# Kernel tuning notes

Measured on AMD Instinct MI355X. Metric: run time of the kernel, lower is better.

Reference implementation:

```python
import jax, jax.numpy as jnp
import numpy as np

MIN_NEAR = 0.05
DENSITY_SCALE = 1.0
BOUND = 1.0  # spherical scene bounds radius
GEO = 15


def _density_mlp(x, dW1, db1, dW2, db2, dW3, db3):
    h = jax.nn.relu(x @ dW1 + db1)
    h = jax.nn.relu(h @ dW2 + db2)
    h = h @ dW3 + db3  # [M, 1+GEO]
    sigma = jnp.exp(jnp.clip(h[..., 0], -15.0, 15.0))  # trunc_exp
    return sigma, h[..., 1:]


def _color_mlp(d, geo, cW1, cb1, cW2, cb2, cW3, cb3):
    h = jnp.concatenate([d, geo], axis=-1)
    h = jax.nn.relu(h @ cW1 + cb1)
    h = jax.nn.relu(h @ cW2 + cb2)
    return jax.nn.sigmoid(h @ cW3 + cb3)


def _comp_weights(deltas, sigmas):
    # alpha compositing: w_i = alpha_i * prod_{j<i}(1 - alpha_j)
    alphas = 1.0 - jnp.exp(-deltas * sigmas)
    trans = jnp.cumprod(
        jnp.concatenate([jnp.ones_like(alphas[:, :1]), 1.0 - alphas + 1e-15], axis=-1),
        axis=-1)[:, :-1]
    return alphas * trans


def _sample_pdf(bins, weights, n_samples):
    # deterministic importance resampling (eval mode); bins [N,T-1], weights [N,T-2]
    weights = weights + 1e-5
    pdf = weights / jnp.sum(weights, axis=-1, keepdims=True)
    cdf = jnp.cumsum(pdf, axis=-1)
    cdf = jnp.concatenate([jnp.zeros_like(cdf[:, :1]), cdf], axis=-1)  # [N, T-1]
    u = jnp.linspace(0.5 / n_samples, 1.0 - 0.5 / n_samples, n_samples)
    u = jnp.broadcast_to(u, (bins.shape[0], n_samples))
    inds = jax.vmap(lambda c, uu: jnp.searchsorted(c, uu, side='right'))(cdf, u)
    below = jnp.clip(inds - 1, 0, cdf.shape[-1] - 1)
    above = jnp.clip(inds, 0, cdf.shape[-1] - 1)
    cdf_g0 = jnp.take_along_axis(cdf, below, axis=-1)
    cdf_g1 = jnp.take_along_axis(cdf, above, axis=-1)
    bmax = bins.shape[-1] - 1
    bins_g0 = jnp.take_along_axis(bins, jnp.clip(below, 0, bmax), axis=-1)
    bins_g1 = jnp.take_along_axis(bins, jnp.clip(above, 0, bmax), axis=-1)
    denom = jnp.where(cdf_g1 - cdf_g0 < 1e-5, 1.0, cdf_g1 - cdf_g0)
    t = (u - cdf_g0) / denom
    return bins_g0 + t * (bins_g1 - bins_g0)


def _run(rays_o, rays_d, dW1, db1, dW2, db2, dW3, db3,
         cW1, cb1, cW2, cb2, cW3, cb3, num_steps, upsample_steps):
    N = rays_o.shape[0]
    # get_z_val_bounds: ray/sphere intersection, sphere radius BOUND at origin
    b = jnp.sum(rays_o * rays_d, axis=-1)
    c = jnp.sum(rays_o * rays_o, axis=-1) - BOUND ** 2
    disc = jnp.maximum(b * b - c, 0.0)
    z_max = jnp.maximum(-b + jnp.sqrt(disc), MIN_NEAR + 1e-3)
    z_min = jnp.full_like(z_max, MIN_NEAR)
    # get_foreground_z_vals: per-ray linspace (perturb=False)
    t = jnp.linspace(0.0, 1.0, num_steps)
    z_vals = z_min[:, None] + (z_max - z_min)[:, None] * t[None, :]
    z_vals = jnp.clip(z_vals, z_min[:, None], z_max[:, None])
    xyzs = rays_o[:, None, :] + rays_d[:, None, :] * z_vals[..., None]
    sigma, geo = _density_mlp(xyzs.reshape(-1, 3), dW1, db1, dW2, db2, dW3, db3)
    sigma = sigma.reshape(N, num_steps)
    geo = geo.reshape(N, num_steps, GEO)

    # upsample_z_values: importance resampling from coarse weights
    deltas = z_vals[:, 1:] - z_vals[:, :-1]
    aug = jnp.concatenate([deltas, deltas[:, -1:]], axis=-1)
    w_coarse = _comp_weights(aug, DENSITY_SCALE * sigma)
    z_mid = 0.5 * (z_vals[:, :-1] + z_vals[:, 1:])
    new_z = jax.lax.stop_gradient(_sample_pdf(z_mid, w_coarse[:, 1:-1], upsample_steps))
    new_xyzs = rays_o[:, None, :] + rays_d[:, None, :] * new_z[..., None]
    new_sigma, new_geo = _density_mlp(new_xyzs.reshape(-1, 3), dW1, db1, dW2, db2, dW3, db3)
    new_sigma = new_sigma.reshape(N, upsample_steps)
    new_geo = new_geo.reshape(N, upsample_steps, GEO)

    # sort/gather merge of coarse + fine samples
    z_all = jnp.concatenate([z_vals, new_z], axis=1)
    order = jnp.argsort(z_all, axis=1)
    z_vals = jnp.take_along_axis(z_all, order, axis=1)  # [N, T]
    xyzs = jnp.take_along_axis(jnp.concatenate([xyzs, new_xyzs], axis=1), order[..., None], axis=1)
    sigma = jnp.take_along_axis(jnp.concatenate([sigma, new_sigma], axis=1), order, axis=1)
    geo = jnp.take_along_axis(jnp.concatenate([geo, new_geo], axis=1), order[..., None], axis=1)

    deltas = z_vals[:, 1:] - z_vals[:, :-1]
    aug = jnp.concatenate([deltas, deltas[:, -1:]], axis=-1)
    weights = _comp_weights(aug, DENSITY_SCALE * sigma)  # [N, T]

    mask = weights > 1e-4
    dirs = jnp.broadcast_to(rays_d[:, None, :], xyzs.shape).reshape(-1, 3)
    rgb = _color_mlp(dirs, geo.reshape(-1, GEO), cW1, cb1, cW2, cb2, cW3, cb3)
    rgbs = jnp.where(mask.reshape(-1, 1), rgb, 0.0).reshape(N, -1, 3)

    weights_sum = jnp.sum(weights, axis=-1)
    depth = jnp.sum(weights * z_vals, axis=-1)
    image = jnp.sum(weights[..., None] * rgbs, axis=-2)
    bg = 206.0 / 255.0
    image = image + (1.0 - weights_sum)[..., None] * bg

    # pairwise distortion loss (the (z_shifted - z_shifted) term in the source is identically zero)
    sample_dist = 1.0 / num_steps
    z_shift = jnp.concatenate([z_vals[:, 1:], jnp.full((N, 1), sample_dist, z_vals.dtype)], axis=-1)
    mid_zs = 0.5 * z_vals + 0.5 * z_shift
    pair = jnp.abs(mid_zs[:, None, :] - mid_zs[:, :, None]) * (weights[:, None, :] * weights[:, :, None])
    loss = jnp.sum(pair, axis=(1, 2)) / (depth + 1e-6)
    loss = jnp.where(loss < 1e-3, 0.0, loss)  # cutoff
    return jnp.concatenate([image, depth[:, None], loss[:, None]], axis=-1)  # [N, 5]


def setup_inputs() -> dict:
    key = jax.random.key(0)
    ks = jax.random.split(key, 16)
    N, H = 2048, 256
    rays_o = 0.1 * jax.random.normal(ks[0], (N, 3), jnp.float32)  # near scene centre
    rd = jax.random.normal(ks[1], (N, 3), jnp.float32)
    rays_d = rd / jnp.linalg.norm(rd, axis=-1, keepdims=True)

    def w(k, shape):
        return jax.random.normal(k, shape, jnp.float32) * (1.0 / np.sqrt(shape[0]))

    return {
        'rays_o': rays_o, 'rays_d': rays_d,
        'dW1': w(ks[2], (3, H)), 'db1': jnp.zeros(H, jnp.float32),
        'dW2': w(ks[3], (H, H)), 'db2': jnp.zeros(H, jnp.float32),
        'dW3': w(ks[4], (H, 1 + GEO)), 'db3': jnp.zeros(1 + GEO, jnp.float32),
        'cW1': w(ks[5], (3 + GEO, H)), 'cb1': jnp.zeros(H, jnp.float32),
        'cW2': w(ks[6], (H, H)), 'cb2': jnp.zeros(H, jnp.float32),
        'cW3': w(ks[7], (H, 3)), 'cb3': jnp.zeros(3, jnp.float32),
        'num_steps': 128, 'upsample_steps': 128,
    }


def reference(rays_o, rays_d, dW1, db1, dW2, db2, dW3, db3,
              cW1, cb1, cW2, cb2, cW3, cb3, num_steps, upsample_steps):
    return _run(rays_o, rays_d, dW1, db1, dW2, db2, dW3, db3,
                cW1, cb1, cW2, cb2, cW3, cb3, num_steps, upsample_steps)
```

## Files before the change

kernel.cpp:

```cpp
#include <hip/hip_runtime.h>


typedef float f32x4 __attribute__((ext_vector_type(4)));
typedef __bf16 bf16x8 __attribute__((ext_vector_type(8)));
typedef __bf16 bf16x4 __attribute__((ext_vector_type(4)));
typedef unsigned short u16x8 __attribute__((ext_vector_type(8)));
typedef unsigned short u16x4 __attribute__((ext_vector_type(4)));

#define NRAYS 2048
#define NSTEP 128
#define TSAMP 256
#define MIN_NEAR 0.05f
#define DTPW 4

#define OFF_D1 0
#define OFF_D2 8192
#define OFF_D3 73728
#define OFF_C1 77824
#define OFF_C2 86016
#define OFF_C3 151552
#define PACK_TOTAL 155648

__device__ __forceinline__ unsigned short f2bf(float f) {
  __bf16 h = (__bf16)f;
  return __builtin_bit_cast(unsigned short, h);
}
__device__ __forceinline__ u16x4 pack4(float a, float b, float c, float d) {
  bf16x4 h;
  h[0] = (__bf16)a; h[1] = (__bf16)b; h[2] = (__bf16)c; h[3] = (__bf16)d;
  return __builtin_bit_cast(u16x4, h);
}

__device__ __forceinline__ float ray_z(const float* __restrict__ ro,
                                       const float* __restrict__ rd, int r, int i) {
  float ox = ro[r * 3], oy = ro[r * 3 + 1], oz = ro[r * 3 + 2];
  float dx = rd[r * 3], dy = rd[r * 3 + 1], dz = rd[r * 3 + 2];
  float b = ox * dx + oy * dy + oz * dz;
  float c = ox * ox + oy * oy + oz * oz - 1.0f;
  float disc = fmaxf(b * b - c, 0.0f);
  float zmax = fmaxf(-b + sqrtf(disc), MIN_NEAR + 1e-3f);
  float zmin = MIN_NEAR;
  float tt = (float)i / 127.0f;
  float zz = zmin + (zmax - zmin) * tt;
  return fminf(fmaxf(zz, zmin), zmax);
}

__device__ __forceinline__ void pack_std(const float* __restrict__ W,
                                         unsigned short* __restrict__ dst,
                                         int idx, int K, int Norig, int NT) {
  int per = NT * 512;
  int kt = idx / per, rm = idx % per;
  int nt = rm >> 9, lane = (rm >> 3) & 63, j = rm & 7;
  int k = kt * 32 + ((lane >> 4) << 3) + j;
  int n = nt * 16 + (lane & 15);
  float v = (k < K && n < Norig) ? W[k * Norig + n] : 0.0f;
  dst[idx] = f2bf(v);
}

__global__ void k_pack_all(const float* __restrict__ dW1, const float* __restrict__ dW2,
                           const float* __restrict__ dW3, const float* __restrict__ cW1,
                           const float* __restrict__ cW2, const float* __restrict__ cW3,
                           unsigned short* __restrict__ Wp) {
  int idx = blockIdx.x * 256 + threadIdx.x;
  if (idx < OFF_D2) {
    pack_std(dW1, Wp + OFF_D1, idx - OFF_D1, 3, 256, 16);
  } else if (idx < OFF_D3) {
    pack_std(dW2, Wp + OFF_D2, idx - OFF_D2, 256, 256, 16);
  } else if (idx < OFF_C1) {
    int j2 = idx - OFF_D3;
    int lane = (j2 >> 3) & 63, jj = j2 & 7, kt = j2 >> 9;
    int k = kt * 32 + ((lane >> 4) << 3) + jj;
    int n = lane & 15;
    Wp[idx] = f2bf(dW3[k * 16 + ((n + 1) & 15)]);
  } else if (idx < OFF_C2) {
    int j2 = idx - OFF_C1;
    int nt = j2 >> 9, lane = (j2 >> 3) & 63, jj = j2 & 7;
    int k = ((lane >> 4) << 3) + jj;
    int n = nt * 16 + (lane & 15);
    float v = 0.0f;
    if (k < 15) v = cW1[(3 + k) * 256 + n];
    else if (k >= 16 && k < 19) v = cW1[(k - 16) * 256 + n];
    Wp[idx] = f2bf(v);
  } else if (idx < OFF_C3) {
    pack_std(cW2, Wp + OFF_C2, idx - OFF_C2, 256, 256, 16);
  } else if (idx < PACK_TOTAL) {
    pack_std(cW3, Wp + OFF_C3, idx - OFF_C3, 256, 3, 1);
  }
}


__device__ __forceinline__ void mlp_l1(const unsigned short* xb, unsigned short* buf,
                                       const bf16x8 (&w1r)[4], const float* sb1,
                                       int wid, int quad, int col) {
#pragma unroll
  for (int h = 0; h < 2; ++h) {
    f32x4 acc[8];
#pragma unroll
    for (int i = 0; i < 8; ++i) acc[i] = (f32x4){0.f, 0.f, 0.f, 0.f};
    int p0 = (h * 2) * 16 + col, p1 = (h * 2 + 1) * 16 + col;
    bf16x8 x0 = *reinterpret_cast<const bf16x8*>(&xb[p0 * 32 + ((quad ^ (p0 & 3)) * 8)]);
    bf16x8 x1 = *reinterpret_cast<const bf16x8*>(&xb[p1 * 32 + ((quad ^ (p1 & 3)) * 8)]);
#pragma unroll
    for (int ntl = 0; ntl < 4; ++ntl) {
      acc[ntl * 2 + 0] = __builtin_amdgcn_mfma_f32_16x16x32_bf16(w1r[ntl], x0, acc[ntl * 2 + 0], 0, 0, 0);
      acc[ntl * 2 + 1] = __builtin_amdgcn_mfma_f32_16x16x32_bf16(w1r[ntl], x1, acc[ntl * 2 + 1], 0, 0, 0);
    }
#pragma unroll
    for (int ntl = 0; ntl < 4; ++ntl) {
      int n = (wid * 4 + ntl) * 16 + quad * 4;
      f32x4 bv = *reinterpret_cast<const f32x4*>(&sb1[n]);
#pragma unroll
      for (int j = 0; j < 2; ++j) {
        int p = (h * 2 + j) * 16 + col;
        *reinterpret_cast<u16x4*>(&buf[p * 256 + (((n >> 3) ^ (p & 31)) * 8) + (n & 7)]) =
            pack4(fmaxf(acc[ntl * 2 + j][0] + bv[0], 0.0f),
                  fmaxf(acc[ntl * 2 + j][1] + bv[1], 0.0f),
                  fmaxf(acc[ntl * 2 + j][2] + bv[2], 0.0f),
                  fmaxf(acc[ntl * 2 + j][3] + bv[3], 0.0f));
      }
    }
  }
}

__device__ __forceinline__ void l2_half_compute(const unsigned short* buf,
                                                const bf16x8 (&w2r)[8][4],
                                                f32x4 (&acc)[8], int h, int quad, int col) {
#pragma unroll
  for (int i = 0; i < 8; ++i) acc[i] = (f32x4){0.f, 0.f, 0.f, 0.f};
#pragma unroll
  for (int kt = 0; kt < 8; ++kt) {
    int p0 = (h * 2) * 16 + col, p1 = (h * 2 + 1) * 16 + col;
    bf16x8 x0 = *reinterpret_cast<const bf16x8*>(&buf[p0 * 256 + (((kt * 4 + quad) ^ (p0 & 31)) * 8)]);
    bf16x8 x1 = *reinterpret_cast<const bf16x8*>(&buf[p1 * 256 + (((kt * 4 + quad) ^ (p1 & 31)) * 8)]);
#pragma unroll
    for (int ntl = 0; ntl < 4; ++ntl) {
      acc[ntl * 2 + 0] = __builtin_amdgcn_mfma_f32_16x16x32_bf16(w2r[kt][ntl], x0, acc[ntl * 2 + 0], 0, 0, 0);
      acc[ntl * 2 + 1] = __builtin_amdgcn_mfma_f32_16x16x32_bf16(w2r[kt][ntl], x1, acc[ntl * 2 + 1], 0, 0, 0);
    }
  }
}

__device__ __forceinline__ void l2_half_write(unsigned short* buf, const f32x4 (&acc)[8],
                                              const float* sb2, int h, int wid, int quad, int col) {
#pragma unroll
  for (int ntl = 0; ntl < 4; ++ntl) {
    int n = (wid * 4 + ntl) * 16 + quad * 4;
    f32x4 bv = *reinterpret_cast<const f32x4*>(&sb2[n]);
#pragma unroll
    for (int j = 0; j < 2; ++j) {
      int p = (h * 2 + j) * 16 + col;
      *reinterpret_cast<u16x4*>(&buf[p * 256 + (((n >> 3) ^ (p & 31)) * 8) + (n & 7)]) =
          pack4(fmaxf(acc[ntl * 2 + j][0] + bv[0], 0.0f),
                fmaxf(acc[ntl * 2 + j][1] + bv[1], 0.0f),
                fmaxf(acc[ntl * 2 + j][2] + bv[2], 0.0f),
                fmaxf(acc[ntl * 2 + j][3] + bv[3], 0.0f));
    }
  }
}

template <bool FIRST>
__global__ __launch_bounds__(256, 2)
void k_density(const float* __restrict__ ro, const float* __restrict__ rd,
               const float* __restrict__ zin,
               const unsigned short* __restrict__ Wp1, const float* __restrict__ b1,
               const unsigned short* __restrict__ Wp2, const float* __restrict__ b2,
               const unsigned short* __restrict__ Wp3, const float* __restrict__ b3,
               unsigned short* __restrict__ gout, float* __restrict__ sig,
               float* __restrict__ z_f) {
  __shared__ __align__(16) unsigned short buf[64 * 256];
  __shared__ unsigned short xb[64 * 32];
  __shared__ unsigned short sW3[4096];
  __shared__ __align__(16) float sb1[256];
  __shared__ __align__(16) float sb2[256];
  __shared__ float sb3[16];
  __shared__ float ssig[256];
  const int t = threadIdx.x;
  const int lane = t & 63, wid = t >> 6, quad = lane >> 4, col = lane & 15;
  const int p_ = t >> 2, g_ = t & 3;

  sb1[t] = b1[t];
  sb2[t] = b2[t];
  if (t < 16) sb3[t] = b3[(t + 1) & 15];
  { const u16x8* s = (const u16x8*)Wp3; u16x8* d = (u16x8*)sW3;
    d[t] = s[t]; d[t + 256] = s[t + 256]; }

  bf16x8 w1r[4], w2r[8][4];
#pragma unroll
  for (int ntl = 0; ntl < 4; ++ntl)
    w1r[ntl] = *reinterpret_cast<const bf16x8*>(Wp1 + ((wid * 4 + ntl) * 64 + lane) * 8);
#pragma unroll
  for (int kt = 0; kt < 8; ++kt)
#pragma unroll
    for (int ntl = 0; ntl < 4; ++ntl)
      w2r[kt][ntl] = *reinterpret_cast<const bf16x8*>(Wp2 + ((kt * 16 + wid * 4 + ntl) * 64 + lane) * 8);

#pragma unroll 1
  for (int tt = 0; tt < DTPW; ++tt) {
    const int P0 = blockIdx.x * 256 + tt * 64;
    {
      u16x8 pk = {0, 0, 0, 0, 0, 0, 0, 0};
      if (g_ == 0) {
        int P = P0 + p_;
        int rr_ = P >> 7, ii = P & 127;
        float zz;
        if constexpr (FIRST) zz = ray_z(ro, rd, rr_, ii);
        else zz = zin[P];
        pk[0] = f2bf(ro[rr_ * 3 + 0] + rd[rr_ * 3 + 0] * zz);
        pk[1] = f2bf(ro[rr_ * 3 + 1] + rd[rr_ * 3 + 1] * zz);
        pk[2] = f2bf(ro[rr_ * 3 + 2] + rd[rr_ * 3 + 2] * zz);
      }
      *reinterpret_cast<u16x8*>(&xb[p_ * 32 + ((g_ ^ (p_ & 3)) * 8)]) = pk;
    }
    __syncthreads();
    mlp_l1(xb, buf, w1r, sb1, wid, quad, col);
    __syncthreads();
    f32x4 acc[8];
    l2_half_compute(buf, w2r, acc, 0, quad, col);
    __syncthreads();
    l2_half_write(buf, acc, sb2, 0, wid, quad, col);
    l2_half_compute(buf, w2r, acc, 1, quad, col);
    __syncthreads();
    l2_half_write(buf, acc, sb2, 1, wid, quad, col);
    __syncthreads();
    {
      const int p = wid * 16 + col;
      f32x4 a3 = {0.f, 0.f, 0.f, 0.f};
#pragma unroll
      for (int kt = 0; kt < 8; ++kt) {
        bf16x8 w = *reinterpret_cast<const bf16x8*>(&sW3[(kt * 64 + lane) * 8]);
        bf16x8 x = *reinterpret_cast<const bf16x8*>(&buf[p * 256 + (((kt * 4 + quad) ^ (p & 31)) * 8)]);
        a3 = __builtin_amdgcn_mfma_f32_16x16x32_bf16(w, x, a3, 0, 0, 0);
      }
      int n0 = quad * 4;
      float v0 = a3[0] + sb3[n0], v1 = a3[1] + sb3[n0 + 1];
      float v2 = a3[2] + sb3[n0 + 2], v3 = a3[3] + sb3[n0 + 3];
      if (quad == 3) {
        float sgm = expf(fminf(fmaxf(v3, -15.f), 15.f));
        sig[P0 + p] = sgm;
        ssig[tt * 64 + p] = sgm;
        v3 = 0.0f;
      }
      *reinterpret_cast<u16x4*>(gout + (size_t)(P0 + p) * 16 + n0) = pack4(v0, v1, v2, v3);
    }
  }

  if constexpr (FIRST) {
    __syncthreads();
    float* pf = reinterpret_cast<float*>(buf);
    float* psz = pf;          float* psl = pf + 256;
    float* psw = pf + 512;    float* pcdf = pf + 768;
    float* pmid = pf + 1024;
    const int seg = (t >> 7) * 128;
    const int i = t & 127;
    const int rg = blockIdx.x * 2 + (t >> 7);
    float zi = ray_z(ro, rd, rg, i);
    psz[seg + i] = zi;
    float sgv = ssig[t];
    __syncthreads();
    float aug = (i < 127) ? psz[seg + i + 1] - zi : psz[seg + 127] - psz[seg + 126];
    float alpha = 1.0f - expf(-aug * sgv);
    psl[seg + i] = logf(1.0f - alpha + 1e-15f);
    __syncthreads();
    for (int off = 1; off < 128; off <<= 1) {
      float y = (i >= off) ? psl[seg + i - off] : 0.0f;
      __syncthreads();
      psl[seg + i] += y;
      __syncthreads();
    }
    float excl = (i > 0) ? psl[seg + i - 1] : 0.0f;
    float w = alpha * expf(excl);
    psw[seg + i] = w;
    __syncthreads();
    float v = (i < 126) ? psw[seg + i + 1] + 1e-5f : 0.0f;
    psl[seg + i] = v;
    __syncthreads();
    for (int off = 1; off < 128; off <<= 1) {
      float y = (i >= off) ? psl[seg + i - off] : 0.0f;
      __syncthreads();
      psl[seg + i] += y;
      __syncthreads();
    }
    float total = psl[seg + 125];
    if (i <= 126) pcdf[seg + i] = (i == 0) ? 0.0f : psl[seg + i - 1] / total;
    if (i < 127) pmid[seg + i] = 0.5f * (psz[seg + i] + psz[seg + i + 1]);
    __syncthreads();
    const float lo = 0.5f / 128.0f, hi = 1.0f - 0.5f / 128.0f;
    float u = lo + (hi - lo) * ((float)i / 127.0f);
    int loI = 0, hiI = 127;
    while (loI < hiI) {
      int mid = (loI + hiI) >> 1;
      if (pcdf[seg + mid] > u) hiI = mid; else loI = mid + 1;
    }
    int below = loI - 1; if (below < 0) below = 0; if (below > 126) below = 126;
    int above = loI;     if (above > 126) above = 126;
    float c0 = pcdf[seg + below], c1 = pcdf[seg + above];
    float b0v = pmid[seg + below], b1v = pmid[seg + above];
    float dn = c1 - c0; if (dn < 1e-5f) dn = 1.0f;
    float ttt = (u - c0) / dn;
    z_f[rg * NSTEP + i] = b0v + ttt * (b1v - b0v);
  }
}

__device__ __forceinline__ float block_reduce(float v, float* s, int t) {
  s[t] = v;
  __syncthreads();
  for (int off = 128; off > 0; off >>= 1) {
    if (t < off) s[t] += s[t + off];
    __syncthreads();
  }
  float r = s[0];
  __syncthreads();
  return r;
}

__global__ __launch_bounds__(256, 2)
void k_mcf(const float* __restrict__ ro, const float* __restrict__ rd,
           const float* __restrict__ z_f,
           const float* __restrict__ sigc, const float* __restrict__ sigf,
           const unsigned short* __restrict__ goutc, const unsigned short* __restrict__ goutf,
           const unsigned short* __restrict__ Wp1, const float* __restrict__ cb1,
           const unsigned short* __restrict__ Wp2, const float* __restrict__ cb2,
           const unsigned short* __restrict__ Wp3, const float* __restrict__ cb3,
           float* __restrict__ out) {
  __shared__ __align__(16) unsigned short buf[64 * 256];
  __shared__ unsigned short xb[64 * 32];
  __shared__ unsigned short sW3[4096];
  __shared__ __align__(16) float sb1[256];
  __shared__ __align__(16) float sb2[256];
  __shared__ float szm[256], swgt[256], smid[256], sred[256], sl[256];
  __shared__ float szc[128], szf[128];
  __shared__ float srgb[3 * 256];
  __shared__ int sord[256];
  const int t = threadIdx.x;
  const int lane = t & 63, wid = t >> 6, quad = lane >> 4, col = lane & 15;
  const int p_ = t >> 2, g_ = t & 3;
  const int r = blockIdx.x;

  sb1[t] = cb1[t];
  sb2[t] = cb2[t];
  { const u16x8* s = (const u16x8*)Wp3; u16x8* d = (u16x8*)sW3;
    d[t] = s[t]; d[t + 256] = s[t + 256]; }

  bf16x8 w1r[4], w2r[8][4];
#pragma unroll
  for (int ntl = 0; ntl < 4; ++ntl)
    w1r[ntl] = *reinterpret_cast<const bf16x8*>(Wp1 + ((wid * 4 + ntl) * 64 + lane) * 8);
#pragma unroll
  for (int kt = 0; kt < 8; ++kt)
#pragma unroll
    for (int ntl = 0; ntl < 4; ++ntl)
      w2r[kt][ntl] = *reinterpret_cast<const bf16x8*>(Wp2 + ((kt * 16 + wid * 4 + ntl) * 64 + lane) * 8);

  if (t < 128) szc[t] = ray_z(ro, rd, r, t);
  else szf[t - 128] = z_f[r * NSTEP + (t - 128)];
  __syncthreads();
  int pos; float myz;
  if (t < 128) {
    myz = szc[t];
    int lo = 0, hi = 128;
    while (lo < hi) { int m = (lo + hi) >> 1; if (szf[m] < myz) lo = m + 1; else hi = m; }
    pos = t + lo;
  } else {
    int j = t - 128; myz = szf[j];
    int lo = 0, hi = 128;
    while (lo < hi) { int m = (lo + hi) >> 1; if (szc[m] <= myz) lo = m + 1; else hi = m; }
    pos = j + lo;
  }
  szm[pos] = myz; sord[pos] = t;
  __syncthreads();
  int src = sord[t];
  float sg = (src < 128) ? sigc[r * NSTEP + src] : sigf[r * NSTEP + (src - 128)];
  float zt = szm[t];
  float aug = (t < 255) ? szm[t + 1] - zt : szm[255] - szm[254];
  float alpha = 1.0f - expf(-aug * sg);
  sl[t] = logf(1.0f - alpha + 1e-15f);
  __syncthreads();
  for (int off = 1; off < 256; off <<= 1) {
    float y = (t >= off) ? sl[t - off] : 0.0f;
    __syncthreads();
    sl[t] += y;
    __syncthreads();
  }
  float excl = (t > 0) ? sl[t - 1] : 0.0f;
  swgt[t] = alpha * expf(excl);

  float dx0 = rd[r * 3], dx1 = rd[r * 3 + 1], dx2 = rd[r * 3 + 2];
  __syncthreads();
  u16x8 gx = {0, 0, 0, 0, 0, 0, 0, 0};
  float wgtv = 0.0f;
  {
    if (g_ < 2) {
      int s0 = sord[p_];
      const unsigned short* gs = (s0 < 128)
          ? (goutc + (size_t)(r * NSTEP + s0) * 16)
          : (goutf + (size_t)(r * NSTEP + (s0 - 128)) * 16);
      gx = *reinterpret_cast<const u16x8*>(gs + g_ * 8);
    } else if (g_ == 2) {
      gx[0] = f2bf(dx0); gx[1] = f2bf(dx1); gx[2] = f2bf(dx2);
    } else {
      wgtv = swgt[p_];
    }
  }
#pragma unroll 1
  for (int tt = 0; tt < 4; ++tt) {
    const int P0l = tt * 64;
    const int haveNext = (tt < 3);
    int go = __syncthreads_or((g_ == 3) && (wgtv > 1e-4f));
    u16x8 gxn = {0, 0, 0, 0, 0, 0, 0, 0};
    float wgtn = 0.0f; int ordn = 0;
    if (go) {
      *reinterpret_cast<u16x8*>(&xb[p_ * 32 + ((g_ ^ (p_ & 3)) * 8)]) = gx;
      __syncthreads();
      mlp_l1(xb, buf, w1r, sb1, wid, quad, col);
      __syncthreads();
    }
    if (haveNext) {
      int Pn = P0l + 64 + p_;
      if (g_ < 2) ordn = sord[Pn];
      else if (g_ == 2) { gxn[0] = f2bf(dx0); gxn[1] = f2bf(dx1); gxn[2] = f2bf(dx2); }
      else wgtn = swgt[Pn];
    }
    f32x4 acc[8];
    if (go) {
      l2_half_compute(buf, w2r, acc, 0, quad, col);
      __syncthreads();
      l2_half_write(buf, acc, sb2, 0, wid, quad, col);
    }
    if (haveNext && g_ < 2) {
      const unsigned short* gs = (ordn < 128)
          ? (goutc + (size_t)(r * NSTEP + ordn) * 16)
          : (goutf + (size_t)(r * NSTEP + (ordn - 128)) * 16);
      gxn = *reinterpret_cast<const u16x8*>(gs + g_ * 8);
    }
    if (go) {
      l2_half_compute(buf, w2r, acc, 1, quad, col);
      __syncthreads();
      l2_half_write(buf, acc, sb2, 1, wid, quad, col);
      __syncthreads();
      {
        const int p = wid * 16 + col;
        f32x4 a3 = {0.f, 0.f, 0.f, 0.f};
#pragma unroll
        for (int kt = 0; kt < 8; ++kt) {
          bf16x8 w = *reinterpret_cast<const bf16x8*>(&sW3[(kt * 64 + lane) * 8]);
          bf16x8 x = *reinterpret_cast<const bf16x8*>(&buf[p * 256 + (((kt * 4 + quad) ^ (p & 31)) * 8)]);
          a3 = __builtin_amdgcn_mfma_f32_16x16x32_bf16(w, x, a3, 0, 0, 0);
        }
        if (quad == 0) {
          int pi = P0l + p;
          srgb[pi * 3 + 0] = 1.0f / (1.0f + expf(-(a3[0] + cb3[0])));
          srgb[pi * 3 + 1] = 1.0f / (1.0f + expf(-(a3[1] + cb3[1])));
          srgb[pi * 3 + 2] = 1.0f / (1.0f + expf(-(a3[2] + cb3[2])));
        }
      }
    }
    gx = gxn; wgtv = wgtn;
  }

  __syncthreads();
  float ztf = szm[t], wtf = swgt[t];
  float znext = (t < 255) ? szm[t + 1] : (1.0f / 128.0f);
  smid[t] = 0.5f * ztf + 0.5f * znext;
  float cr = 0.f, cg = 0.f, cbv = 0.f;
  if (wtf > 1e-4f) {
    cr = srgb[t * 3]; cg = srgb[t * 3 + 1]; cbv = srgb[t * 3 + 2];
  }
  __syncthreads();
  float mt = smid[t];
  float accl = 0.f;
  for (int j = 0; j < 256; ++j) accl += fabsf(mt - smid[j]) * swgt[j];
  accl *= wtf;
  float wsum = block_reduce(wtf, sred, t);
  float depth = block_reduce(wtf * ztf, sred, t);
  float ir = block_reduce(wtf * cr, sred, t);
  float ig = block_reduce(wtf * cg, sred, t);
  float ib = block_reduce(wtf * cbv, sred, t);
  float S = block_reduce(accl, sred, t);
  if (t == 0) {
    const float bgc = 206.0f / 255.0f;
    float loss = S / (depth + 1e-6f);
    if (loss < 1e-3f) loss = 0.0f;
    out[r * 5 + 0] = ir + (1.0f - wsum) * bgc;
    out[r * 5 + 1] = ig + (1.0f - wsum) * bgc;
    out[r * 5 + 2] = ib + (1.0f - wsum) * bgc;
    out[r * 5 + 3] = depth;
    out[r * 5 + 4] = loss;
  }
}

extern "C" void kernel_launch(void* const* d_in, const int* in_sizes, int n_in,
                              void* d_out, int out_size, void* d_ws, size_t ws_size,
                              hipStream_t stream) {
  const float* rays_o = (const float*)d_in[0];
  const float* rays_d = (const float*)d_in[1];
  const float* dW1 = (const float*)d_in[2];
  const float* db1 = (const float*)d_in[3];
  const float* dW2 = (const float*)d_in[4];
  const float* db2 = (const float*)d_in[5];
  const float* dW3 = (const float*)d_in[6];
  const float* db3 = (const float*)d_in[7];
  const float* cW1 = (const float*)d_in[8];
  const float* cb1 = (const float*)d_in[9];
  const float* cW2 = (const float*)d_in[10];
  const float* cb2 = (const float*)d_in[11];
  const float* cW3 = (const float*)d_in[12];
  const float* cb3 = (const float*)d_in[13];

  char* ws = (char*)d_ws;
  size_t off = 0;
  auto alloc = [&](size_t bytes) -> void* {
    void* p = ws + off;
    off += (bytes + 255) & ~(size_t)255;
    return p;
  };
  unsigned short* Wp = (unsigned short*)alloc((size_t)PACK_TOTAL * 2);
  unsigned short* goutc = (unsigned short*)alloc((size_t)NRAYS * NSTEP * 16 * 2);
  unsigned short* goutf = (unsigned short*)alloc((size_t)NRAYS * NSTEP * 16 * 2);
  float* sigc = (float*)alloc((size_t)NRAYS * NSTEP * 4);
  float* sigf = (float*)alloc((size_t)NRAYS * NSTEP * 4);
  float* z_f  = (float*)alloc((size_t)NRAYS * NSTEP * 4);
  (void)ws_size; (void)in_sizes; (void)n_in; (void)out_size;

  k_pack_all<<<PACK_TOTAL / 256, 256, 0, stream>>>(dW1, dW2, dW3, cW1, cW2, cW3, Wp);

  k_density<true><<<(NRAYS * NSTEP) / 256, 256, 0, stream>>>(
      rays_o, rays_d, nullptr,
      Wp + OFF_D1, db1, Wp + OFF_D2, db2, Wp + OFF_D3, db3, goutc, sigc, z_f);
  k_density<false><<<(NRAYS * NSTEP) / 256, 256, 0, stream>>>(
      rays_o, rays_d, z_f,
      Wp + OFF_D1, db1, Wp + OFF_D2, db2, Wp + OFF_D3, db3, goutf, sigf, nullptr);
  k_mcf<<<NRAYS, 256, 0, stream>>>(
      rays_o, rays_d, z_f, sigc, sigf, goutc, goutf,
      Wp + OFF_C1, cb1, Wp + OFF_C2, cb2, Wp + OFF_C3, cb3, (float*)d_out);
}
```

Baseline: 289.0 us.

## Double-buffer MLP activations, replace LDS scans with wave shuffles, linearize distortion loss

Splits the activation buffer into ping-pong A/B buffers so layer 2 needs no mid-layer barriers. Layer-1 inputs now stay in registers instead of passing through a staging buffer. Barrier-heavy shared-memory Hillis-Steele scans and tree reductions become wave shuffle scans and reductions. The O(N^2) distortion-loss loop becomes a prefix-sum formula. Next-tile gathers are prefetched, and fast __expf/__logf intrinsics are used; this doubles LDS use (occupancy risk) and slightly changes numerics.

```diff
diff --git a/kernel.cpp b/kernel.cpp
--- a/kernel.cpp
+++ b/kernel.cpp
@@ -9,9 +9,7 @@
 
 #define NRAYS 2048
 #define NSTEP 128
-#define TSAMP 256
 #define MIN_NEAR 0.05f
-#define DTPW 4
 
 #define OFF_D1 0
 #define OFF_D2 8192
@@ -31,18 +29,37 @@
   return __builtin_bit_cast(u16x4, h);
 }
 
-__device__ __forceinline__ float ray_z(const float* __restrict__ ro,
-                                       const float* __restrict__ rd, int r, int i) {
+__device__ __forceinline__ float ray_zmax(const float* __restrict__ ro,
+                                          const float* __restrict__ rd, int r) {
   float ox = ro[r * 3], oy = ro[r * 3 + 1], oz = ro[r * 3 + 2];
   float dx = rd[r * 3], dy = rd[r * 3 + 1], dz = rd[r * 3 + 2];
   float b = ox * dx + oy * dy + oz * dz;
   float c = ox * ox + oy * oy + oz * oz - 1.0f;
   float disc = fmaxf(b * b - c, 0.0f);
-  float zmax = fmaxf(-b + sqrtf(disc), MIN_NEAR + 1e-3f);
-  float zmin = MIN_NEAR;
-  float tt = (float)i / 127.0f;
-  float zz = zmin + (zmax - zmin) * tt;
-  return fminf(fmaxf(zz, zmin), zmax);
+  return fmaxf(-b + sqrtf(disc), MIN_NEAR + 1e-3f);
+}
+__device__ __forceinline__ float z_at(float zmax, int i) {
+  float zz = MIN_NEAR + (zmax - MIN_NEAR) * ((float)i / 127.0f);
+  return fminf(fmaxf(zz, MIN_NEAR), zmax);
+}
+
+__device__ __forceinline__ float wave_iscan(float v, int lane) {
+#pragma unroll
+  for (int off = 1; off < 64; off <<= 1) {
+    float y = __shfl_up(v, off, 64);
+    if (lane >= off) v += y;
+  }
+  return v;
+}
+__device__ __forceinline__ float block_iscan(float v, float* part, int lane, int wid) {
+  float s = wave_iscan(v, lane);
+  if (lane == 63) part[wid] = s;
+  __syncthreads();
+  float pre = 0.f;
+  if (wid > 0) pre += part[0];
+  if (wid > 1) pre += part[1];
+  if (wid > 2) pre += part[2];
+  return s + pre;
 }
 
 __device__ __forceinline__ void pack_std(const float* __restrict__ W,
@@ -89,21 +106,18 @@
 }
 
 
-__device__ __forceinline__ void mlp_l1(const unsigned short* xb, unsigned short* buf,
-                                       const bf16x8 (&w1r)[4], const float* sb1,
-                                       int wid, int quad, int col) {
+__device__ __forceinline__ void mlp_l1_reg(const bf16x8 (&x)[4], unsigned short* dst,
+                                           const bf16x8 (&w1r)[4], const float* sb1,
+                                           int wid, int quad, int col) {
 #pragma unroll
   for (int h = 0; h < 2; ++h) {
     f32x4 acc[8];
 #pragma unroll
     for (int i = 0; i < 8; ++i) acc[i] = (f32x4){0.f, 0.f, 0.f, 0.f};
-    int p0 = (h * 2) * 16 + col, p1 = (h * 2 + 1) * 16 + col;
-    bf16x8 x0 = *reinterpret_cast<const bf16x8*>(&xb[p0 * 32 + ((quad ^ (p0 & 3)) * 8)]);
-    bf16x8 x1 = *reinterpret_cast<const bf16x8*>(&xb[p1 * 32 + ((quad ^ (p1 & 3)) * 8)]);
 #pragma unroll
     for (int ntl = 0; ntl < 4; ++ntl) {
-      acc[ntl * 2 + 0] = __builtin_amdgcn_mfma_f32_16x16x32_bf16(w1r[ntl], x0, acc[ntl * 2 + 0], 0, 0, 0);
-      acc[ntl * 2 + 1] = __builtin_amdgcn_mfma_f32_16x16x32_bf16(w1r[ntl], x1, acc[ntl * 2 + 1], 0, 0, 0);
+      acc[ntl * 2 + 0] = __builtin_amdgcn_mfma_f32_16x16x32_bf16(w1r[ntl], x[h * 2 + 0], acc[ntl * 2 + 0], 0, 0, 0);
+      acc[ntl * 2 + 1] = __builtin_amdgcn_mfma_f32_16x16x32_bf16(w1r[ntl], x[h * 2 + 1], acc[ntl * 2 + 1], 0, 0, 0);
     }
 #pragma unroll
     for (int ntl = 0; ntl < 4; ++ntl) {
@@ -112,36 +126,31 @@
 #pragma unroll
       for (int j = 0; j < 2; ++j) {
         int p = (h * 2 + j) * 16 + col;
-        *reinterpret_cast<u16x4*>(&buf[p * 256 + (((n >> 3) ^ (p & 31)) * 8) + (n & 7)]) =
-            pack4(fmaxf(acc[ntl * 2 + j][0] + bv[0], 0.0f),
-                  fmaxf(acc[ntl * 2 + j][1] + bv[1], 0.0f),
-                  fmaxf(acc[ntl * 2 + j][2] + bv[2], 0.0f),
-                  fmaxf(acc[ntl * 2 + j][3] + bv[3], 0.0f));
-      }
-    }
-  }
-}
-
-__device__ __forceinline__ void l2_half_compute(const unsigned short* buf,
-                                                const bf16x8 (&w2r)[8][4],
-                                                f32x4 (&acc)[8], int h, int quad, int col) {
+        *reinterpret_cast<u16x4*>(&dst[p * 256 + (((n >> 3) ^ (p & 31)) * 8) + (n & 7)]) =
+            pack4(fmaxf(acc[ntl * 2 + j][0] + bv[0], 0.f), fmaxf(acc[ntl * 2 + j][1] + bv[1], 0.f),
+                  fmaxf(acc[ntl * 2 + j][2] + bv[2], 0.f), fmaxf(acc[ntl * 2 + j][3] + bv[3], 0.f));
+      }
+    }
+  }
+}
+
+__device__ __forceinline__ void l2_pass(const unsigned short* src, unsigned short* dst,
+                                        const bf16x8 (&w2r)[8][4], const float* sb2,
+                                        int h, int wid, int quad, int col) {
+  f32x4 acc[8];
 #pragma unroll
   for (int i = 0; i < 8; ++i) acc[i] = (f32x4){0.f, 0.f, 0.f, 0.f};
+  const int p0 = (h * 2) * 16 + col, p1 = (h * 2 + 1) * 16 + col;
 #pragma unroll
   for (int kt = 0; kt < 8; ++kt) {
-    int p0 = (h * 2) * 16 + col, p1 = (h * 2 + 1) * 16 + col;
-    bf16x8 x0 = *reinterpret_cast<const bf16x8*>(&buf[p0 * 256 + (((kt * 4 + quad) ^ (p0 & 31)) * 8)]);
-    bf16x8 x1 = *reinterpret_cast<const bf16x8*>(&buf[p1 * 256 + (((kt * 4 + quad) ^ (p1 & 31)) * 8)]);
+    bf16x8 x0 = *reinterpret_cast<const bf16x8*>(&src[p0 * 256 + (((kt * 4 + quad) ^ (p0 & 31)) * 8)]);
+    bf16x8 x1 = *reinterpret_cast<const bf16x8*>(&src[p1 * 256 + (((kt * 4 + quad) ^ (p1 & 31)) * 8)]);
 #pragma unroll
     for (int ntl = 0; ntl < 4; ++ntl) {
       acc[ntl * 2 + 0] = __builtin_amdgcn_mfma_f32_16x16x32_bf16(w2r[kt][ntl], x0, acc[ntl * 2 + 0], 0, 0, 0);
       acc[ntl * 2 + 1] = __builtin_amdgcn_mfma_f32_16x16x32_bf16(w2r[kt][ntl], x1, acc[ntl * 2 + 1], 0, 0, 0);
     }
   }
-}
-
-__device__ __forceinline__ void l2_half_write(unsigned short* buf, const f32x4 (&acc)[8],
-                                              const float* sb2, int h, int wid, int quad, int col) {
 #pragma unroll
   for (int ntl = 0; ntl < 4; ++ntl) {
     int n = (wid * 4 + ntl) * 16 + quad * 4;
@@ -149,11 +158,9 @@
 #pragma unroll
     for (int j = 0; j < 2; ++j) {
       int p = (h * 2 + j) * 16 + col;
-      *reinterpret_cast<u16x4*>(&buf[p * 256 + (((n >> 3) ^ (p & 31)) * 8) + (n & 7)]) =
-          pack4(fmaxf(acc[ntl * 2 + j][0] + bv[0], 0.0f),
-                fmaxf(acc[ntl * 2 + j][1] + bv[1], 0.0f),
-                fmaxf(acc[ntl * 2 + j][2] + bv[2], 0.0f),
-                fmaxf(acc[ntl * 2 + j][3] + bv[3], 0.0f));
+      *reinterpret_cast<u16x4*>(&dst[p * 256 + (((n >> 3) ^ (p & 31)) * 8) + (n & 7)]) =
+          pack4(fmaxf(acc[ntl * 2 + j][0] + bv[0], 0.f), fmaxf(acc[ntl * 2 + j][1] + bv[1], 0.f),
+                fmaxf(acc[ntl * 2 + j][2] + bv[2], 0.f), fmaxf(acc[ntl * 2 + j][3] + bv[3], 0.f));
     }
   }
 }
@@ -167,16 +174,16 @@
                const unsigned short* __restrict__ Wp3, const float* __restrict__ b3,
                unsigned short* __restrict__ gout, float* __restrict__ sig,
                float* __restrict__ z_f) {
-  __shared__ __align__(16) unsigned short buf[64 * 256];
-  __shared__ unsigned short xb[64 * 32];
-  __shared__ unsigned short sW3[4096];
+  __shared__ __align__(16) unsigned short bufA[64 * 256];
+  __shared__ __align__(16) unsigned short bufB[64 * 256];
+  __shared__ __align__(16) unsigned short sW3[4096];
   __shared__ __align__(16) float sb1[256];
   __shared__ __align__(16) float sb2[256];
-  __shared__ float sb3[16];
-  __shared__ float ssig[256];
+  __shared__ __align__(16) float sb3[16];
+  __shared__ __align__(16) float ssig[256];
+  __shared__ __align__(16) float sred[16];
   const int t = threadIdx.x;
   const int lane = t & 63, wid = t >> 6, quad = lane >> 4, col = lane & 15;
-  const int p_ = t >> 2, g_ = t & 3;
 
   sb1[t] = b1[t];
   sb2[t] = b2[t];
@@ -194,33 +201,53 @@
     for (int ntl = 0; ntl < 4; ++ntl)
       w2r[kt][ntl] = *reinterpret_cast<const bf16x8*>(Wp2 + ((kt * 16 + wid * 4 + ntl) * 64 + lane) * 8);
 
+  const int rg0 = blockIdx.x * 2;
+  float zmax0 = ray_zmax(ro, rd, rg0);
+  float zmax1 = ray_zmax(ro, rd, rg0 + 1);
+  float oax = ro[rg0 * 3], oay = ro[rg0 * 3 + 1], oaz = ro[rg0 * 3 + 2];
+  float dax = rd[rg0 * 3], day = rd[rg0 * 3 + 1], daz = rd[rg0 * 3 + 2];
+  float obx = ro[rg0 * 3 + 3], oby = ro[rg0 * 3 + 4], obz = ro[rg0 * 3 + 5];
+  float dbx = rd[rg0 * 3 + 3], dby = rd[rg0 * 3 + 4], dbz = rd[rg0 * 3 + 5];
+
+  float zv[4] = {0.f, 0.f, 0.f, 0.f};
+  if constexpr (!FIRST) {
+    if (quad == 0) {
+#pragma unroll
+      for (int pt = 0; pt < 4; ++pt) zv[pt] = zin[blockIdx.x * 256 + pt * 16 + col];
+    }
+  }
+  __syncthreads();
+
 #pragma unroll 1
-  for (int tt = 0; tt < DTPW; ++tt) {
+  for (int tt = 0; tt < 4; ++tt) {
     const int P0 = blockIdx.x * 256 + tt * 64;
-    {
-      u16x8 pk = {0, 0, 0, 0, 0, 0, 0, 0};
-      if (g_ == 0) {
-        int P = P0 + p_;
-        int rr_ = P >> 7, ii = P & 127;
+    bf16x8 x[4];
+#pragma unroll
+    for (int pt = 0; pt < 4; ++pt) {
+      u16x8 raw = {0, 0, 0, 0, 0, 0, 0, 0};
+      if (quad == 0) {
+        int p = pt * 16 + col;
+        int P = P0 + p;
+        int hi = (P >> 7) & 1;
         float zz;
-        if constexpr (FIRST) zz = ray_z(ro, rd, rr_, ii);
-        else zz = zin[P];
-        pk[0] = f2bf(ro[rr_ * 3 + 0] + rd[rr_ * 3 + 0] * zz);
-        pk[1] = f2bf(ro[rr_ * 3 + 1] + rd[rr_ * 3 + 1] * zz);
-        pk[2] = f2bf(ro[rr_ * 3 + 2] + rd[rr_ * 3 + 2] * zz);
-      }
-      *reinterpret_cast<u16x8*>(&xb[p_ * 32 + ((g_ ^ (p_ & 3)) * 8)]) = pk;
-    }
-    __syncthreads();
-    mlp_l1(xb, buf, w1r, sb1, wid, quad, col);
-    __syncthreads();
-    f32x4 acc[8];
-    l2_half_compute(buf, w2r, acc, 0, quad, col);
-    __syncthreads();
-    l2_half_write(buf, acc, sb2, 0, wid, quad, col);
-    l2_half_compute(buf, w2r, acc, 1, quad, col);
-    __syncthreads();
-    l2_half_write(buf, acc, sb2, 1, wid, quad, col);
+        if constexpr (FIRST) zz = z_at(hi ? zmax1 : zmax0, P & 127);
+        else zz = zv[pt];
+        raw[0] = f2bf((hi ? obx : oax) + (hi ? dbx : dax) * zz);
+        raw[1] = f2bf((hi ? oby : oay) + (hi ? dby : day) * zz);
+        raw[2] = f2bf((hi ? obz : oaz) + (hi ? dbz : daz) * zz);
+      }
+      x[pt] = __builtin_bit_cast(bf16x8, raw);
+    }
+    if constexpr (!FIRST) {
+      if (tt < 3 && quad == 0) {
+#pragma unroll
+        for (int pt = 0; pt < 4; ++pt) zv[pt] = zin[P0 + 64 + pt * 16 + col];
+      }
+    }
+    mlp_l1_reg(x, bufA, w1r, sb1, wid, quad, col);
+    __syncthreads();
+    l2_pass(bufA, bufB, w2r, sb2, 0, wid, quad, col);
+    l2_pass(bufA, bufB, w2r, sb2, 1, wid, quad, col);
     __syncthreads();
     {
       const int p = wid * 16 + col;
@@ -228,16 +255,16 @@
 #pragma unroll
       for (int kt = 0; kt < 8; ++kt) {
         bf16x8 w = *reinterpret_cast<const bf16x8*>(&sW3[(kt * 64 + lane) * 8]);
-        bf16x8 x = *reinterpret_cast<const bf16x8*>(&buf[p * 256 + (((kt * 4 + quad) ^ (p & 31)) * 8)]);
-        a3 = __builtin_amdgcn_mfma_f32_16x16x32_bf16(w, x, a3, 0, 0, 0);
+        bf16x8 xx = *reinterpret_cast<const bf16x8*>(&bufB[p * 256 + (((kt * 4 + quad) ^ (p & 31)) * 8)]);
+        a3 = __builtin_amdgcn_mfma_f32_16x16x32_bf16(w, xx, a3, 0, 0, 0);
       }
       int n0 = quad * 4;
       float v0 = a3[0] + sb3[n0], v1 = a3[1] + sb3[n0 + 1];
       float v2 = a3[2] + sb3[n0 + 2], v3 = a3[3] + sb3[n0 + 3];
       if (quad == 3) {
-        float sgm = expf(fminf(fmaxf(v3, -15.f), 15.f));
+        float sgm = __expf(fminf(fmaxf(v3, -15.f), 15.f));
         sig[P0 + p] = sgm;
-        ssig[tt * 64 + p] = sgm;
+        if constexpr (FIRST) ssig[tt * 64 + p] = sgm;
         v3 = 0.0f;
       }
       *reinterpret_cast<u16x4*>(gout + (size_t)(P0 + p) * 16 + n0) = pack4(v0, v1, v2, v3);
@@ -246,43 +273,37 @@
 
   if constexpr (FIRST) {
     __syncthreads();
-    float* pf = reinterpret_cast<float*>(buf);
-    float* psz = pf;          float* psl = pf + 256;
-    float* psw = pf + 512;    float* pcdf = pf + 768;
-    float* pmid = pf + 1024;
-    const int seg = (t >> 7) * 128;
+    float* psz = reinterpret_cast<float*>(bufA);
+    float* pmid = psz + 256;
+    float* pcdf = psz + 512;
+    float* psw = psz + 768;
+    const int segw = t >> 7;
     const int i = t & 127;
-    const int rg = blockIdx.x * 2 + (t >> 7);
-    float zi = ray_z(ro, rd, rg, i);
+    const int seg = segw * 128;
+    float zi = z_at(segw ? zmax1 : zmax0, i);
     psz[seg + i] = zi;
     float sgv = ssig[t];
     __syncthreads();
     float aug = (i < 127) ? psz[seg + i + 1] - zi : psz[seg + 127] - psz[seg + 126];
-    float alpha = 1.0f - expf(-aug * sgv);
-    psl[seg + i] = logf(1.0f - alpha + 1e-15f);
-    __syncthreads();
-    for (int off = 1; off < 128; off <<= 1) {
-      float y = (i >= off) ? psl[seg + i - off] : 0.0f;
-      __syncthreads();
-      psl[seg + i] += y;
-      __syncthreads();
-    }
-    float excl = (i > 0) ? psl[seg + i - 1] : 0.0f;
-    float w = alpha * expf(excl);
+    float alpha = 1.0f - __expf(-aug * sgv);
+    float lt = __logf(1.0f - alpha + 1e-15f);
+    float s = wave_iscan(lt, lane);
+    if (lane == 63) sred[wid] = s;
+    __syncthreads();
+    if (wid & 1) s += sred[wid - 1];
+    float w = alpha * __expf(s - lt);
     psw[seg + i] = w;
-    __syncthreads();
-    float v = (i < 126) ? psw[seg + i + 1] + 1e-5f : 0.0f;
-    psl[seg + i] = v;
-    __syncthreads();
-    for (int off = 1; off < 128; off <<= 1) {
-      float y = (i >= off) ? psl[seg + i - off] : 0.0f;
-      __syncthreads();
-      psl[seg + i] += y;
-      __syncthreads();
-    }
-    float total = psl[seg + 125];
-    if (i <= 126) pcdf[seg + i] = (i == 0) ? 0.0f : psl[seg + i - 1] / total;
-    if (i < 127) pmid[seg + i] = 0.5f * (psz[seg + i] + psz[seg + i + 1]);
+    if (i < 127) pmid[seg + i] = 0.5f * (zi + psz[seg + i + 1]);
+    __syncthreads();
+    float v2s = (i < 126) ? psw[seg + i + 1] + 1e-5f : 0.f;
+    float s2 = wave_iscan(v2s, lane);
+    if (lane == 63) sred[8 + wid] = s2;
+    __syncthreads();
+    if (wid & 1) s2 += sred[8 + wid - 1];
+    psw[seg + i] = s2;
+    __syncthreads();
+    float total = psw[seg + 125];
+    if (i <= 126) pcdf[seg + i] = (i == 0) ? 0.f : psw[seg + i - 1] / total;
     __syncthreads();
     const float lo = 0.5f / 128.0f, hi = 1.0f - 0.5f / 128.0f;
     float u = lo + (hi - lo) * ((float)i / 127.0f);
@@ -297,20 +318,8 @@
     float b0v = pmid[seg + below], b1v = pmid[seg + above];
     float dn = c1 - c0; if (dn < 1e-5f) dn = 1.0f;
     float ttt = (u - c0) / dn;
-    z_f[rg * NSTEP + i] = b0v + ttt * (b1v - b0v);
-  }
-}
-
-__device__ __forceinline__ float block_reduce(float v, float* s, int t) {
-  s[t] = v;
-  __syncthreads();
-  for (int off = 128; off > 0; off >>= 1) {
-    if (t < off) s[t] += s[t + off];
-    __syncthreads();
-  }
-  float r = s[0];
-  __syncthreads();
-  return r;
+    z_f[(rg0 + segw) * NSTEP + i] = b0v + ttt * (b1v - b0v);
+  }
 }
 
 __global__ __launch_bounds__(256, 2)
@@ -322,18 +331,18 @@
            const unsigned short* __restrict__ Wp2, const float* __restrict__ cb2,
            const unsigned short* __restrict__ Wp3, const float* __restrict__ cb3,
            float* __restrict__ out) {
-  __shared__ __align__(16) unsigned short buf[64 * 256];
-  __shared__ unsigned short xb[64 * 32];
-  __shared__ unsigned short sW3[4096];
+  __shared__ __align__(16) unsigned short bufA[64 * 256];
+  __shared__ __align__(16) unsigned short bufB[64 * 256];
+  __shared__ __align__(16) unsigned short sW3[4096];
   __shared__ __align__(16) float sb1[256];
   __shared__ __align__(16) float sb2[256];
-  __shared__ float szm[256], swgt[256], smid[256], sred[256], sl[256];
-  __shared__ float szc[128], szf[128];
-  __shared__ float srgb[3 * 256];
-  __shared__ int sord[256];
+  __shared__ __align__(16) float szm[256];
+  __shared__ __align__(16) float swgt[256];
+  __shared__ __align__(16) float srgb[768];
+  __shared__ __align__(16) float sred[48];
+  __shared__ unsigned short sord[256];
   const int t = threadIdx.x;
   const int lane = t & 63, wid = t >> 6, quad = lane >> 4, col = lane & 15;
-  const int p_ = t >> 2, g_ = t & 3;
   const int r = blockIdx.x;
 
   sb1[t] = cb1[t];
@@ -351,7 +360,10 @@
     for (int ntl = 0; ntl < 4; ++ntl)
       w2r[kt][ntl] = *reinterpret_cast<const bf16x8*>(Wp2 + ((kt * 16 + wid * 4 + ntl) * 64 + lane) * 8);
 
-  if (t < 128) szc[t] = ray_z(ro, rd, r, t);
+  float* szc = reinterpret_cast<float*>(bufA);
+  float* szf = szc + 128;
+  float zmaxr = ray_zmax(ro, rd, r);
+  if (t < 128) szc[t] = z_at(zmaxr, t);
   else szf[t - 128] = z_f[r * NSTEP + (t - 128)];
   __syncthreads();
   int pos; float myz;
@@ -366,76 +378,51 @@
     while (lo < hi) { int m = (lo + hi) >> 1; if (szc[m] <= myz) lo = m + 1; else hi = m; }
     pos = j + lo;
   }
-  szm[pos] = myz; sord[pos] = t;
-  __syncthreads();
-  int src = sord[t];
-  float sg = (src < 128) ? sigc[r * NSTEP + src] : sigf[r * NSTEP + (src - 128)];
+  szm[pos] = myz; sord[pos] = (unsigned short)t;
+  __syncthreads();
+  int srci = sord[t];
+  float sg = (srci < 128) ? sigc[r * NSTEP + srci] : sigf[r * NSTEP + (srci - 128)];
   float zt = szm[t];
   float aug = (t < 255) ? szm[t + 1] - zt : szm[255] - szm[254];
-  float alpha = 1.0f - expf(-aug * sg);
-  sl[t] = logf(1.0f - alpha + 1e-15f);
-  __syncthreads();
-  for (int off = 1; off < 256; off <<= 1) {
-    float y = (t >= off) ? sl[t - off] : 0.0f;
-    __syncthreads();
-    sl[t] += y;
-    __syncthreads();
-  }
-  float excl = (t > 0) ? sl[t - 1] : 0.0f;
-  swgt[t] = alpha * expf(excl);
-
-  float dx0 = rd[r * 3], dx1 = rd[r * 3 + 1], dx2 = rd[r * 3 + 2];
-  __syncthreads();
-  u16x8 gx = {0, 0, 0, 0, 0, 0, 0, 0};
-  float wgtv = 0.0f;
-  {
-    if (g_ < 2) {
-      int s0 = sord[p_];
-      const unsigned short* gs = (s0 < 128)
-          ? (goutc + (size_t)(r * NSTEP + s0) * 16)
-          : (goutf + (size_t)(r * NSTEP + (s0 - 128)) * 16);
-      gx = *reinterpret_cast<const u16x8*>(gs + g_ * 8);
-    } else if (g_ == 2) {
-      gx[0] = f2bf(dx0); gx[1] = f2bf(dx1); gx[2] = f2bf(dx2);
-    } else {
-      wgtv = swgt[p_];
-    }
-  }
+  float alpha = 1.0f - __expf(-aug * sg);
+  float lt = __logf(1.0f - alpha + 1e-15f);
+  float incl = block_iscan(lt, sred, lane, wid);
+  swgt[t] = alpha * __expf(incl - lt);
+  __syncthreads();
+
+  float dv0 = rd[r * 3], dv1 = rd[r * 3 + 1], dv2 = rd[r * 3 + 2];
+  u16x8 dirpk = {f2bf(dv0), f2bf(dv1), f2bf(dv2), 0, 0, 0, 0, 0};
+  u16x8 gx[4], gxn[4];
+  auto gather = [&](int tile, u16x8 (&g)[4]) {
+    if (quad < 2) {
+#pragma unroll
+      for (int pt = 0; pt < 4; ++pt) {
+        int p = pt * 16 + col;
+        int s = sord[tile * 64 + p];
+        const unsigned short* gs = ((s < 128) ? goutc : goutf)
+            + ((size_t)(r * NSTEP + (s & 127)) * 16) + quad * 8;
+        g[pt] = *reinterpret_cast<const u16x8*>(gs);
+      }
+    }
+  };
+  gather(0, gx);
 #pragma unroll 1
   for (int tt = 0; tt < 4; ++tt) {
-    const int P0l = tt * 64;
-    const int haveNext = (tt < 3);
-    int go = __syncthreads_or((g_ == 3) && (wgtv > 1e-4f));
-    u16x8 gxn = {0, 0, 0, 0, 0, 0, 0, 0};
-    float wgtn = 0.0f; int ordn = 0;
+    int pred = swgt[tt * 64 + (t & 63)] > 1e-4f;
+    int go = __syncthreads_or(pred);
+    if (tt < 3) gather(tt + 1, gxn);
     if (go) {
-      *reinterpret_cast<u16x8*>(&xb[p_ * 32 + ((g_ ^ (p_ & 3)) * 8)]) = gx;
+      bf16x8 x[4];
+#pragma unroll
+      for (int pt = 0; pt < 4; ++pt) {
+        u16x8 raw = (quad < 2) ? gx[pt]
+                  : ((quad == 2) ? dirpk : (u16x8){0, 0, 0, 0, 0, 0, 0, 0});
+        x[pt] = __builtin_bit_cast(bf16x8, raw);
+      }
+      mlp_l1_reg(x, bufA, w1r, sb1, wid, quad, col);
       __syncthreads();
-      mlp_l1(xb, buf, w1r, sb1, wid, quad, col);
-      __syncthreads();
-    }
-    if (haveNext) {
-      int Pn = P0l + 64 + p_;
-      if (g_ < 2) ordn = sord[Pn];
-      else if (g_ == 2) { gxn[0] = f2bf(dx0); gxn[1] = f2bf(dx1); gxn[2] = f2bf(dx2); }
-      else wgtn = swgt[Pn];
-    }
-    f32x4 acc[8];
-    if (go) {
-      l2_half_compute(buf, w2r, acc, 0, quad, col);
-      __syncthreads();
-      l2_half_write(buf, acc, sb2, 0, wid, quad, col);
-    }
-    if (haveNext && g_ < 2) {
-      const unsigned short* gs = (ordn < 128)
-          ? (goutc + (size_t)(r * NSTEP + ordn) * 16)
-          : (goutf + (size_t)(r * NSTEP + (ordn - 128)) * 16);
-      gxn = *reinterpret_cast<const u16x8*>(gs + g_ * 8);
-    }
-    if (go) {
-      l2_half_compute(buf, w2r, acc, 1, quad, col);
-      __syncthreads();
-      l2_half_write(buf, acc, sb2, 1, wid, quad, col);
+      l2_pass(bufA, bufB, w2r, sb2, 0, wid, quad, col);
+      l2_pass(bufA, bufB, w2r, sb2, 1, wid, quad, col);
       __syncthreads();
       {
         const int p = wid * 16 + col;
@@ -443,46 +430,61 @@
 #pragma unroll
         for (int kt = 0; kt < 8; ++kt) {
           bf16x8 w = *reinterpret_cast<const bf16x8*>(&sW3[(kt * 64 + lane) * 8]);
-          bf16x8 x = *reinterpret_cast<const bf16x8*>(&buf[p * 256 + (((kt * 4 + quad) ^ (p & 31)) * 8)]);
-          a3 = __builtin_amdgcn_mfma_f32_16x16x32_bf16(w, x, a3, 0, 0, 0);
+          bf16x8 xx = *reinterpret_cast<const bf16x8*>(&bufB[p * 256 + (((kt * 4 + quad) ^ (p & 31)) * 8)]);
+          a3 = __builtin_amdgcn_mfma_f32_16x16x32_bf16(w, xx, a3, 0, 0, 0);
         }
         if (quad == 0) {
-          int pi = P0l + p;
-          srgb[pi * 3 + 0] = 1.0f / (1.0f + expf(-(a3[0] + cb3[0])));
-          srgb[pi * 3 + 1] = 1.0f / (1.0f + expf(-(a3[1] + cb3[1])));
-          srgb[pi * 3 + 2] = 1.0f / (1.0f + expf(-(a3[2] + cb3[2])));
+          int pi = tt * 64 + p;
+          srgb[pi * 3 + 0] = 1.0f / (1.0f + __expf(-(a3[0] + cb3[0])));
+          srgb[pi * 3 + 1] = 1.0f / (1.0f + __expf(-(a3[1] + cb3[1])));
+          srgb[pi * 3 + 2] = 1.0f / (1.0f + __expf(-(a3[2] + cb3[2])));
         }
       }
     }
-    gx = gxn; wgtv = wgtn;
+    if (tt < 3) {
+#pragma unroll
+      for (int pt = 0; pt < 4; ++pt) gx[pt] = gxn[pt];
+    }
   }
 
   __syncthreads();
   float ztf = szm[t], wtf = swgt[t];
   float znext = (t < 255) ? szm[t + 1] : (1.0f / 128.0f);
-  smid[t] = 0.5f * ztf + 0.5f * znext;
-  float cr = 0.f, cg = 0.f, cbv = 0.f;
-  if (wtf > 1e-4f) {
-    cr = srgb[t * 3]; cg = srgb[t * 3 + 1]; cbv = srgb[t * 3 + 2];
-  }
-  __syncthreads();
-  float mt = smid[t];
-  float accl = 0.f;
-  for (int j = 0; j < 256; ++j) accl += fabsf(mt - smid[j]) * swgt[j];
-  accl *= wtf;
-  float wsum = block_reduce(wtf, sred, t);
-  float depth = block_reduce(wtf * ztf, sred, t);
-  float ir = block_reduce(wtf * cr, sred, t);
-  float ig = block_reduce(wtf * cg, sred, t);
-  float ib = block_reduce(wtf * cbv, sred, t);
-  float S = block_reduce(accl, sred, t);
+  float mt = 0.5f * ztf + 0.5f * znext;
+  float cr = 0.f, cg = 0.f, cbl = 0.f;
+  if (wtf > 1e-4f) { cr = srgb[t * 3]; cg = srgb[t * 3 + 1]; cbl = srgb[t * 3 + 2]; }
+  if (t == 255) { sred[36] = mt; sred[37] = wtf; }
+  float wm = (t < 255) ? wtf : 0.f;
+  float Pw = block_iscan(wm, sred, lane, wid);
+  float Ps = block_iscan(wm * mt, sred + 4, lane, wid);
+  float W254 = sred[0] + sred[1] + sred[2] + sred[3];
+  float S254 = sred[4] + sred[5] + sred[6] + sred[7];
+  float m255 = sred[36], w255 = sred[37];
+  float contrib = 0.f;
+  if (t < 255)
+    contrib = wtf * (mt * (2.f * Pw - W254) - (2.f * Ps - S254))
+            + 2.f * wtf * fabsf(mt - m255) * w255;
+  float vals[6] = {wtf, wtf * ztf, wtf * cr, wtf * cg, wtf * cbl, contrib};
+#pragma unroll
+  for (int k = 0; k < 6; ++k) {
+    float v = vals[k];
+#pragma unroll
+    for (int m = 1; m < 64; m <<= 1) v += __shfl_xor(v, m, 64);
+    if (lane == 0) sred[8 + k * 4 + wid] = v;
+  }
+  __syncthreads();
   if (t == 0) {
+    float a6[6];
+#pragma unroll
+    for (int k = 0; k < 6; ++k)
+      a6[k] = sred[8 + k * 4] + sred[8 + k * 4 + 1] + sred[8 + k * 4 + 2] + sred[8 + k * 4 + 3];
     const float bgc = 206.0f / 255.0f;
-    float loss = S / (depth + 1e-6f);
+    float wsum = a6[0], depth = a6[1];
+    float loss = a6[5] / (depth + 1e-6f);
     if (loss < 1e-3f) loss = 0.0f;
-    out[r * 5 + 0] = ir + (1.0f - wsum) * bgc;
-    out[r * 5 + 1] = ig + (1.0f - wsum) * bgc;
-    out[r * 5 + 2] = ib + (1.0f - wsum) * bgc;
+    out[r * 5 + 0] = a6[2] + (1.0f - wsum) * bgc;
+    out[r * 5 + 1] = a6[3] + (1.0f - wsum) * bgc;
+    out[r * 5 + 2] = a6[4] + (1.0f - wsum) * bgc;
     out[r * 5 + 3] = depth;
     out[r * 5 + 4] = loss;
   }
```

New measurement: 442.5 us. 1.53x slower.
